# Optimization experiments

Hardware: AMD Instinct MI355X
Metric: run time of the kernel (lower is better)

The kernel has to match this reference:

```python
import jax, jax.numpy as jnp
import numpy as np

K = 64                      # sort-pool k
B_GRAPHS, N_PER = 256, 512  # graphs, nodes per graph
DIM_F, E_PER = 128, 8192    # node feature dim, edges per graph
EMB = 32


def setup_inputs() -> dict:
    key = jax.random.key(0)
    ks = jax.random.split(key, 12)
    N = B_GRAPHS * N_PER
    off = (jnp.arange(B_GRAPHS) * N_PER)[:, None]
    x = jax.random.normal(ks[0], (N, DIM_F), jnp.float32)
    edge_src = (jax.random.randint(ks[1], (B_GRAPHS, E_PER), 0, N_PER) + off).reshape(-1)
    edge_dst = (jax.random.randint(ks[2], (B_GRAPHS, E_PER), 0, N_PER) + off).reshape(-1)

    def lin(k, o, i):
        return (jax.random.normal(k, (o, i), jnp.float32) / np.float32(np.sqrt(i)))

    return {
        "x": x,
        "W0": lin(ks[3], EMB, DIM_F), "b0": jnp.zeros((EMB,), jnp.float32),
        "W1": lin(ks[4], EMB, EMB),   "b1": jnp.zeros((EMB,), jnp.float32),
        "W2": lin(ks[5], EMB, EMB),   "b2": jnp.zeros((EMB,), jnp.float32),
        "W3": lin(ks[6], 1, EMB),     "b3": jnp.zeros((1,), jnp.float32),
        "conv1_w": jax.random.normal(ks[7], (16, 1, 97), jnp.float32) / np.float32(np.sqrt(97.0)),
        "conv1_b": jnp.zeros((16,), jnp.float32),
        "conv2_w": jax.random.normal(ks[8], (32, 16, 5), jnp.float32) / np.float32(np.sqrt(80.0)),
        "conv2_b": jnp.zeros((32,), jnp.float32),
        "d1_w": lin(ks[9], 128, 896),  "d1_b": jnp.zeros((128,), jnp.float32),
        "d2_w": lin(ks[10], 10, 128),  "d2_b": jnp.zeros((10,), jnp.float32),
        "edge_src": edge_src, "edge_dst": edge_dst,
        "num_graphs": B_GRAPHS,
    }


def _dgcnn_conv(h_in, W, b, src, dst):
    # h = lin(x); message = (1/deg_src)[dst] * h[src]; scatter-add at dst
    N = h_in.shape[0]
    h = h_in @ W.T + b
    deg = jax.ops.segment_sum(jnp.ones_like(src, dtype=h.dtype), src, num_segments=N)
    norm = 1.0 / deg                       # self-loops guarantee deg >= 1
    msg = h[src] * norm[dst][:, None]      # [E+N, C]
    return jax.ops.segment_sum(msg, dst, num_segments=N)


def _forward(x, W0, b0, W1, b1, W2, b2, W3, b3,
             conv1_w, conv1_b, conv2_w, conv2_b,
             d1_w, d1_b, d2_w, d2_b, src, dst, num_graphs):
    N = x.shape[0]
    self_idx = jnp.arange(N)
    src = jnp.concatenate([src, self_idx])   # add_self_loops
    dst = jnp.concatenate([dst, self_idx])
    hs = []
    h = x
    for (W, b) in ((W0, b0), (W1, b1), (W2, b2), (W3, b3)):
        h = jnp.tanh(_dgcnn_conv(h, W, b, src, dst))
        hs.append(h)
    feat = jnp.concatenate(hs, axis=1)       # [N, 97]
    D = feat.shape[1]
    B = num_graphs
    n = N // B
    g = feat.reshape(B, n, D)
    # global_sort_pool: sort nodes per graph by last channel, descending, take top-k
    order = jnp.argsort(-g[:, :, -1], axis=1)[:, :K]
    topk = jnp.take_along_axis(g, order[:, :, None], axis=1)   # [B, K, D]
    # Conv1d(1,16,kernel=D,stride=D) over [B,1,K*D] == per-node linear on D
    c1 = jax.nn.relu(jnp.einsum('bkd,od->bok', topk, conv1_w[:, 0, :])
                     + conv1_b[None, :, None])                  # [B,16,K]
    p = c1.reshape(B, 16, K // 2, 2).max(axis=-1)               # MaxPool1d(2,2)
    c2 = jax.lax.conv_general_dilated(p, conv2_w, (1,), 'VALID',
                                      dimension_numbers=('NCH', 'OIH', 'NCH'))
    c2 = jax.nn.relu(c2 + conv2_b[None, :, None])               # [B,32,28]
    flat = c2.reshape(B, -1)                                    # [B,896]
    hid = jax.nn.relu(flat @ d1_w.T + d1_b)                     # dropout = identity (eval)
    return hid @ d2_w.T + d2_b                                  # [B,10]


def reference(x, W0, b0, W1, b1, W2, b2, W3, b3,
              conv1_w, conv1_b, conv2_w, conv2_b,
              d1_w, d1_b, d2_w, d2_b, edge_src, edge_dst, num_graphs):
    return _forward(x, W0, b0, W1, b1, W2, b2, W3, b3,
                    conv1_w, conv1_b, conv2_w, conv2_b,
                    d1_w, d1_b, d2_w, d2_b, edge_src, edge_dst, num_graphs)
```

## Files before the change

### kernel.cpp

```cpp
#include <hip/hip_runtime.h>

#define NG   256
#define NP   512
#define EPG  8192
#define FDIM 128
#define STB  36

#define OFF_STAGE 0
#define OFF_BUFB  65536
#define OFF_CSR   139264
#define OFF_OFFS  155648
#define OFF_WT    156680
#define OFF_CUR   156712
#define OFF_DCNT  158760
#define OFF_NRM   160808
#define SMEM_SZ   162856

#define OFF_KEY   OFF_CSR
#define OFF_RANKP (OFF_CSR + 2048)
#define OFF_TIDX  (OFF_CSR + 4096)
#define OFF_TKEY  (OFF_CSR + 4352)
#define OFF_L3    OFF_CUR
#define FO_FEAT 0
#define FO_C1   6208
#define FO_P    7232
#define FO_C2   7744
#define FO_HID  8640

__global__ __launch_bounds__(1024, 4) void dgcnn_fused(
    const float* __restrict__ x,
    const float* __restrict__ W0, const float* __restrict__ b0,
    const float* __restrict__ W1, const float* __restrict__ b1,
    const float* __restrict__ W2, const float* __restrict__ b2,
    const float* __restrict__ W3, const float* __restrict__ b3,
    const float* __restrict__ c1w, const float* __restrict__ c1b,
    const float* __restrict__ c2w, const float* __restrict__ c2b,
    const float* __restrict__ d1w, const float* __restrict__ d1b,
    const float* __restrict__ d2w, const float* __restrict__ d2b,
    const int* __restrict__ esrc, const int* __restrict__ edst,
    float* __restrict__ hs2,
    float* __restrict__ out)
{
  extern __shared__ char smem[];
  float*          stageF = (float*)(smem + OFF_STAGE);
  float*          bufB  = (float*)(smem + OFF_BUFB);
  unsigned short* csr   = (unsigned short*)(smem + OFF_CSR);
  unsigned short* offs  = (unsigned short*)(smem + OFF_OFFS);
  unsigned int*   wt    = (unsigned int*)(smem + OFF_WT);
  unsigned int*   cur   = (unsigned int*)(smem + OFF_CUR);
  unsigned int*   dcnt  = (unsigned int*)(smem + OFF_DCNT);
  float*          nrm   = (float*)(smem + OFF_NRM);
  float*          lin3S = (float*)(smem + OFF_L3);
  float*          keyA  = (float*)(smem + OFF_KEY);
  unsigned short* rankP = (unsigned short*)(smem + OFF_RANKP);
  unsigned short* topIdx= (unsigned short*)(smem + OFF_TIDX);
  float*          topKey= (float*)(smem + OFF_TKEY);

  const int g    = blockIdx.x;
  const int tid  = threadIdx.x;
  const int lane = tid & 63;
  const int wv   = __builtin_amdgcn_readfirstlane(tid >> 6);
  const int half = __builtin_amdgcn_readfirstlane(tid >> 9);
  const int v    = tid & 511;
  const int nb   = g * NP;

  const int ldRow0 = tid >> 3;
  const int ldGrp  = tid & 7;
  const int ldSwz  = (ldGrp ^ (ldRow0 & 7)) * 16;
  auto load_chunk = [&](int kc, float4* xr) {
    const float* base = x + (size_t)nb * FDIM + kc * 32 + ldGrp * 4;
#pragma unroll
    for (int it = 0; it < 4; it++)
      xr[it] = *(const float4*)(base + (size_t)(ldRow0 + it * 128) * FDIM);
  };
  auto store_chunk = [&](const float4* xr) {
#pragma unroll
    for (int it = 0; it < 4; it++)
      *(float4*)(smem + OFF_STAGE + (ldRow0 + it * 128) * 128 + ldSwz) = xr[it];
  };

  float4 xr[4], xr2[4];
  load_chunk(0, xr);
  const int eb = g * EPG;
  const int4* s4p = (const int4*)(esrc + eb);
  const int4* d4p = (const int4*)(edst + eb);
  const int4 sa = s4p[tid], sb = s4p[tid + 1024];
  const int4 da = d4p[tid], db = d4p[tid + 1024];

  int es[8], ed[8];
  es[0]=sa.x-nb; es[1]=sa.y-nb; es[2]=sa.z-nb; es[3]=sa.w-nb;
  es[4]=sb.x-nb; es[5]=sb.y-nb; es[6]=sb.z-nb; es[7]=sb.w-nb;
  ed[0]=da.x-nb; ed[1]=da.y-nb; ed[2]=da.z-nb; ed[3]=da.w-nb;
  ed[4]=db.x-nb; ed[5]=db.y-nb; ed[6]=db.z-nb; ed[7]=db.w-nb;

  if (tid < 512) { cur[tid] = 0u; dcnt[tid] = 0u; }

  float acc0[16];
#pragma unroll
  for (int c = 0; c < 16; c++) acc0[c] = b0[half * 16 + c];
  const char* rowp = smem + OFF_STAGE + v * 128;
  const int vswz = v & 7;

  auto compute_chunk = [&](const int kc) {
#pragma unroll
    for (int jg = 0; jg < 8; jg++) {
      const float4 t = *(const float4*)(rowp + ((jg ^ vswz) * 16));
#pragma unroll
      for (int c = 0; c < 16; c++) {
        const float* wr = W0 + (size_t)(half * 16 + c) * FDIM + kc * 32 + jg * 4;
        acc0[c] = fmaf(t.x, wr[0], acc0[c]);
        acc0[c] = fmaf(t.y, wr[1], acc0[c]);
        acc0[c] = fmaf(t.z, wr[2], acc0[c]);
        acc0[c] = fmaf(t.w, wr[3], acc0[c]);
      }
    }
  };

  __syncthreads();
  store_chunk(xr);
  load_chunk(1, xr2);
  __syncthreads();
#pragma unroll
  for (int i = 0; i < 8; i++) {
    atomicAdd(&dcnt[es[i]], 1u);
    atomicAdd(&dcnt[ed[i]], 65536u);
  }
  compute_chunk(0);
#pragma unroll
  for (int it = 0; it < 4; it++) xr[it] = xr2[it];
  __syncthreads();
  store_chunk(xr);
  load_chunk(2, xr2);
  __syncthreads();
  unsigned c_scan = 0;
  if (tid < 512) {
    const unsigned cw = dcnt[tid];
    nrm[tid] = 1.0f / (float)((cw & 0xFFFFu) + 1u);
    c_scan = cw >> 16;
    for (int d = 1; d < 64; d <<= 1) {
      const unsigned t = __shfl_up(c_scan, (unsigned)d, 64);
      if (lane >= d) c_scan += t;
    }
    if (lane == 63) wt[wv] = c_scan;
  }
  compute_chunk(1);
#pragma unroll
  for (int it = 0; it < 4; it++) xr[it] = xr2[it];
  __syncthreads();
  store_chunk(xr);
  load_chunk(3, xr2);
  __syncthreads();
  if (tid < 512) {
    unsigned base = 0;
    for (int w = 0; w < wv; w++) base += wt[w];
    offs[tid + 1] = (unsigned short)(base + c_scan);
    if (tid == 0) offs[0] = 0;
  }
  compute_chunk(2);
  __syncthreads();
  store_chunk(xr2);
  __syncthreads();
#pragma unroll
  for (int i = 0; i < 8; i++) {
    const unsigned pos = (unsigned)offs[ed[i]] + atomicAdd(&cur[ed[i]], 1u);
    csr[pos] = (unsigned short)es[i];
  }
  compute_chunk(3);
  {
    float4* br = (float4*)(bufB + v * STB + half * 16);
#pragma unroll
    for (int j = 0; j < 4; j++)
      br[j] = make_float4(acc0[j*4+0], acc0[j*4+1], acc0[j*4+2], acc0[j*4+3]);
  }
  __syncthreads();

  float h[16];
  auto do_agg = [&]() {
    float4 A0, A1, A2, A3;
    const float4* sr = (const float4*)(bufB + v * STB + half * 16);
    A0 = sr[0]; A1 = sr[1]; A2 = sr[2]; A3 = sr[3];
    const int e0 = offs[v], e1 = offs[v + 1];
    int e = e0;
    for (; e + 3 < e1; e += 4) {
      const int s0 = csr[e], s1 = csr[e + 1], s2 = csr[e + 2], s3 = csr[e + 3];
      const float4* rb0 = (const float4*)(bufB + s0 * STB + half * 16);
      const float4* rb1 = (const float4*)(bufB + s1 * STB + half * 16);
      const float4* rb2 = (const float4*)(bufB + s2 * STB + half * 16);
      const float4* rb3 = (const float4*)(bufB + s3 * STB + half * 16);
      const float4 p0 = rb0[0], p1 = rb0[1], p2 = rb0[2], p3 = rb0[3];
      const float4 q0 = rb1[0], q1 = rb1[1], q2 = rb1[2], q3 = rb1[3];
      const float4 r0 = rb2[0], r1 = rb2[1], r2 = rb2[2], r3 = rb2[3];
      const float4 t0 = rb3[0], t1 = rb3[1], t2 = rb3[2], t3 = rb3[3];
      A0.x += p0.x + q0.x; A0.y += p0.y + q0.y; A0.z += p0.z + q0.z; A0.w += p0.w + q0.w;
      A1.x += p1.x + q1.x; A1.y += p1.y + q1.y; A1.z += p1.z + q1.z; A1.w += p1.w + q1.w;
      A2.x += p2.x + q2.x; A2.y += p2.y + q2.y; A2.z += p2.z + q2.z; A2.w += p2.w + q2.w;
      A3.x += p3.x + q3.x; A3.y += p3.y + q3.y; A3.z += p3.z + q3.z; A3.w += p3.w + q3.w;
      A0.x += r0.x + t0.x; A0.y += r0.y + t0.y; A0.z += r0.z + t0.z; A0.w += r0.w + t0.w;
      A1.x += r1.x + t1.x; A1.y += r1.y + t1.y; A1.z += r1.z + t1.z; A1.w += r1.w + t1.w;
      A2.x += r2.x + t2.x; A2.y += r2.y + t2.y; A2.z += r2.z + t2.z; A2.w += r2.w + t2.w;
      A3.x += r3.x + t3.x; A3.y += r3.y + t3.y; A3.z += r3.z + t3.z; A3.w += r3.w + t3.w;
    }
    for (; e + 1 < e1; e += 2) {
      const int s0 = csr[e], s1 = csr[e + 1];
      const float4* rb0 = (const float4*)(bufB + s0 * STB + half * 16);
      const float4* rb1 = (const float4*)(bufB + s1 * STB + half * 16);
      const float4 p0 = rb0[0], p1 = rb0[1], p2 = rb0[2], p3 = rb0[3];
      const float4 q0 = rb1[0], q1 = rb1[1], q2 = rb1[2], q3 = rb1[3];
      A0.x += p0.x + q0.x; A0.y += p0.y + q0.y; A0.z += p0.z + q0.z; A0.w += p0.w + q0.w;
      A1.x += p1.x + q1.x; A1.y += p1.y + q1.y; A1.z += p1.z + q1.z; A1.w += p1.w + q1.w;
      A2.x += p2.x + q2.x; A2.y += p2.y + q2.y; A2.z += p2.z + q2.z; A2.w += p2.w + q2.w;
      A3.x += p3.x + q3.x; A3.y += p3.y + q3.y; A3.z += p3.z + q3.z; A3.w += p3.w + q3.w;
    }
    if (e < e1) {
      const int s = csr[e];
      const float4* rb = (const float4*)(bufB + s * STB + half * 16);
      const float4 r0 = rb[0], r1 = rb[1], r2 = rb[2], r3 = rb[3];
      A0.x += r0.x; A0.y += r0.y; A0.z += r0.z; A0.w += r0.w;
      A1.x += r1.x; A1.y += r1.y; A1.z += r1.z; A1.w += r1.w;
      A2.x += r2.x; A2.y += r2.y; A2.z += r2.z; A2.w += r2.w;
      A3.x += r3.x; A3.y += r3.y; A3.z += r3.z; A3.w += r3.w;
    }
    const float nv = nrm[v];
    h[0]=tanhf(A0.x*nv); h[1]=tanhf(A0.y*nv); h[2]=tanhf(A0.z*nv); h[3]=tanhf(A0.w*nv);
    h[4]=tanhf(A1.x*nv); h[5]=tanhf(A1.y*nv); h[6]=tanhf(A1.z*nv); h[7]=tanhf(A1.w*nv);
    h[8]=tanhf(A2.x*nv); h[9]=tanhf(A2.y*nv); h[10]=tanhf(A2.z*nv); h[11]=tanhf(A2.w*nv);
    h[12]=tanhf(A3.x*nv); h[13]=tanhf(A3.y*nv); h[14]=tanhf(A3.z*nv); h[15]=tanhf(A3.w*nv);
  };

  auto put_h = [&]() {
    float4* br = (float4*)(bufB + v * STB + half * 16);
#pragma unroll
    for (int j = 0; j < 4; j++)
      br[j] = make_float4(h[j*4+0], h[j*4+1], h[j*4+2], h[j*4+3]);
  };

  auto store_h1 = [&]() {
#pragma unroll
    for (int c = 0; c < 16; c++)
      stageF[(half * 16 + c) * 512 + v] = h[c];
  };

  auto spill2 = [&]() {
    float4* dst = (float4*)(hs2 + (size_t)(nb + v) * 32 + half * 16);
#pragma unroll
    for (int j = 0; j < 4; j++)
      dst[j] = make_float4(h[j*4+0], h[j*4+1], h[j*4+2], h[j*4+3]);
  };

  auto do_lin = [&](const float* __restrict__ W, const float* __restrict__ b) {
    float hf[32];
    const float4* rr = (const float4*)(bufB + v * STB);
#pragma unroll
    for (int j = 0; j < 8; j++) {
      const float4 t = rr[j];
      hf[j*4+0]=t.x; hf[j*4+1]=t.y; hf[j*4+2]=t.z; hf[j*4+3]=t.w;
    }
    __syncthreads();
    float acc[16];
#pragma unroll
    for (int c = 0; c < 16; c++) {
      const int C = half * 16 + c;
      const float* wr = W + C * 32;
      float a = b[C];
#pragma unroll
      for (int j = 0; j < 32; j++) a = fmaf(hf[j], wr[j], a);
      acc[c] = a;
    }
    float4* br = (float4*)(bufB + v * STB + half * 16);
#pragma unroll
    for (int j = 0; j < 4; j++)
      br[j] = make_float4(acc[j*4+0], acc[j*4+1], acc[j*4+2], acc[j*4+3]);
    __syncthreads();
  };

  do_agg();
  __syncthreads();
  put_h(); store_h1();
  __syncthreads();
  do_lin(W1, b1);
  do_agg();
  __syncthreads();
  put_h(); spill2();
  __syncthreads();
  do_lin(W2, b2);
  do_agg();
  __syncthreads();
  put_h();
  __syncthreads();

  if (tid < 512) {
    const float4* rr = (const float4*)(bufB + tid * STB);
    double a = (double)b3[0];
#pragma unroll
    for (int j = 0; j < 8; j++) {
      const float4 t = rr[j];
      a = fma((double)t.x, (double)W3[j*4+0], a);
      a = fma((double)t.y, (double)W3[j*4+1], a);
      a = fma((double)t.z, (double)W3[j*4+2], a);
      a = fma((double)t.w, (double)W3[j*4+3], a);
    }
    lin3S[tid] = (float)a;
  }
  __syncthreads();
  float h4 = 0.f;
  if (tid < 512) {
    double a = (double)lin3S[tid];
    const int e0 = offs[tid], e1 = offs[tid + 1];
    for (int e = e0; e < e1; e++) a += (double)lin3S[csr[e]];
    a *= (double)nrm[tid];
    h4 = tanhf((float)a);
  }
  __syncthreads();
  if (tid < 512) keyA[tid] = h4;
  __syncthreads();

  {
    const int i = tid & 511;
    const int p = tid >> 9;
    const float ki = keyA[i];
    const float4* k4 = (const float4*)(keyA + p * 256);
    int cnt = 0;
#pragma unroll 8
    for (int jj = 0; jj < 64; jj++) {
      const float4 kv = k4[jj];
      const int j0 = p * 256 + jj * 4;
      cnt += (kv.x > ki || (kv.x == ki && (j0    ) < i)) ? 1 : 0;
      cnt += (kv.y > ki || (kv.y == ki && (j0 + 1) < i)) ? 1 : 0;
      cnt += (kv.z > ki || (kv.z == ki && (j0 + 2) < i)) ? 1 : 0;
      cnt += (kv.w > ki || (kv.w == ki && (j0 + 3) < i)) ? 1 : 0;
    }
    rankP[tid] = (unsigned short)cnt;
  }
  __syncthreads();
  if (tid < 512) {
    const int r = (int)rankP[tid] + (int)rankP[tid + 512];
    if (r < 64) { topIdx[r] = (unsigned short)tid; topKey[r] = keyA[tid]; }
  }
  __syncthreads();

  {
    const int k = lane;
    const int t = wv;
    const int node = (int)topIdx[k];
    const float a0 = stageF[ t       * 512 + node];
    const float a1 = stageF[(t + 16) * 512 + node];
    const float* h2row = hs2 + (size_t)(nb + node) * 32;
    const float b0v = h2row[t];
    const float b1v = h2row[t + 16];
    const float* brow = bufB + node * STB;
    const float c0v = brow[t];
    const float c1v = brow[t + 16];
    const float kk = topKey[k];
    __syncthreads();
    float* featS = bufB + FO_FEAT;
    featS[ t        * 64 + k] = a0;
    featS[(t + 16)  * 64 + k] = a1;
    featS[(t + 32)  * 64 + k] = b0v;
    featS[(t + 48)  * 64 + k] = b1v;
    featS[(t + 64)  * 64 + k] = c0v;
    featS[(t + 80)  * 64 + k] = c1v;
    if (t == 0) featS[96 * 64 + k] = kk;
  }
  __syncthreads();

  {
    const float* featS = bufB + FO_FEAT;
    float* c1s = bufB + FO_C1;
    const int ch = wv;
    float a = c1b[ch];
    const float* wr = c1w + ch * 97;
    for (int d = 0; d < 97; d++)
      a = fmaf(featS[d * 64 + lane], wr[d], a);
    c1s[ch * 64 + lane] = fmaxf(a, 0.f);
  }
  __syncthreads();

  if (tid < 512) {
    const float* c1s = bufB + FO_C1;
    float* ps  = bufB + FO_P;
    const int o = tid >> 5, jj = tid & 31;
    ps[o * 32 + jj] = fmaxf(c1s[o * 64 + 2 * jj], c1s[o * 64 + 2 * jj + 1]);
  }
  __syncthreads();

  {
    const float* ps  = bufB + FO_P;
    float* c2s = bufB + FO_C2;
    const int o = wv;
    if (lane < 28) {
      float a0 = 0.f, a1 = 0.f;
      for (int i = 0; i < 16; i++) {
#pragma unroll
        for (int r = 0; r < 5; r++) {
          const float pv = ps[i * 32 + lane + r];
          a0 = fmaf(pv, c2w[((o     ) * 16 + i) * 5 + r], a0);
          a1 = fmaf(pv, c2w[((o + 16) * 16 + i) * 5 + r], a1);
        }
      }
      c2s[(o     ) * 28 + lane] = fmaxf(a0 + c2b[o     ], 0.f);
      c2s[(o + 16) * 28 + lane] = fmaxf(a1 + c2b[o + 16], 0.f);
    }
  }
  __syncthreads();

  {
    const float* c2s  = bufB + FO_C2;
    float* hids = bufB + FO_HID;
    float fl[14];
#pragma unroll
    for (int j = 0; j < 14; j++) fl[j] = c2s[lane + j * 64];
#pragma unroll 2
    for (int hh = 0; hh < 8; hh++) {
      const int hI = wv * 8 + hh;
      const float* wr = d1w + (size_t)hI * 896;
      float a = 0.f;
#pragma unroll
      for (int j = 0; j < 14; j++) a = fmaf(fl[j], wr[lane + j * 64], a);
#pragma unroll
      for (int m = 32; m > 0; m >>= 1) a += __shfl_xor(a, m, 64);
      if (lane == 0) hids[hI] = fmaxf(a + d1b[hI], 0.f);
    }
  }
  __syncthreads();

  if (tid < 10) {
    const float* hids = bufB + FO_HID;
    const float* wr = d2w + tid * 128;
    double a = (double)d2b[tid];
#pragma unroll 8
    for (int hh = 0; hh < 128; hh++) a = fma((double)hids[hh], (double)wr[hh], a);
    out[g * 10 + tid] = (float)a;
  }
}

extern "C" void kernel_launch(void* const* d_in, const int* in_sizes, int n_in,
                              void* d_out, int out_size, void* d_ws, size_t ws_size,
                              hipStream_t stream) {
  const float* x   = (const float*)d_in[0];
  const float* W0  = (const float*)d_in[1];
  const float* b0  = (const float*)d_in[2];
  const float* W1  = (const float*)d_in[3];
  const float* b1  = (const float*)d_in[4];
  const float* W2  = (const float*)d_in[5];
  const float* b2  = (const float*)d_in[6];
  const float* W3  = (const float*)d_in[7];
  const float* b3  = (const float*)d_in[8];
  const float* c1w = (const float*)d_in[9];
  const float* c1b = (const float*)d_in[10];
  const float* c2w = (const float*)d_in[11];
  const float* c2b = (const float*)d_in[12];
  const float* d1w = (const float*)d_in[13];
  const float* d1b = (const float*)d_in[14];
  const float* d2w = (const float*)d_in[15];
  const float* d2b = (const float*)d_in[16];
  const int* esrc  = (const int*)d_in[17];
  const int* edst  = (const int*)d_in[18];

  float* hs2 = (float*)d_ws;
  float* outp = (float*)d_out;

  hipFuncSetAttribute(reinterpret_cast<const void*>(dgcnn_fused),
                      hipFuncAttributeMaxDynamicSharedMemorySize, SMEM_SZ);
  dgcnn_fused<<<NG, 1024, SMEM_SZ, stream>>>(x, W0, b0, W1, b1, W2, b2, W3, b3,
                                             c1w, c1b, c2w, c2b, d1w, d1b, d2w, d2b,
                                             esrc, edst, hs2, outp);
}
```

Measured before the change: 281.2 us.

## Drop put_h round trips and barriers; fuse maxpool into conv1 via shuffles

The layer-1 and layer-2 linear steps now read their inputs directly from the transposed stage buffer and from the global hs2 spill, instead of writing them into bufB and reading them back. This removes put_h calls and several __syncthreads. The key buffer is moved to a separate shared-memory region so the final tanh can write it directly, which drops one more barrier. The conv1 ReLU and the MaxPool are combined using wavefront shuffles, which removes the c1 shared-memory buffer and a barrier, at the cost of uncached global reads for the layer-2 input.

```diff
diff --git a/kernel.cpp b/kernel.cpp
--- a/kernel.cpp
+++ b/kernel.cpp
@@ -12,20 +12,20 @@
 #define OFF_OFFS  155648
 #define OFF_WT    156680
 #define OFF_CUR   156712
-#define OFF_DCNT  158760
-#define OFF_NRM   160808
-#define SMEM_SZ   162856
-
-#define OFF_KEY   OFF_CSR
-#define OFF_RANKP (OFF_CSR + 2048)
-#define OFF_TIDX  (OFF_CSR + 4096)
-#define OFF_TKEY  (OFF_CSR + 4352)
+#define OFF_PAD   158760
+#define OFF_DCNT  158768
+#define OFF_NRM   160816
+#define SMEM_SZ   162864
+
 #define OFF_L3    OFF_CUR
+#define OFF_KEY   OFF_DCNT
+#define OFF_RANKP OFF_CSR
+#define OFF_TIDX  (OFF_CSR + 2048)
+#define OFF_TKEY  (OFF_CSR + 2304)
 #define FO_FEAT 0
-#define FO_C1   6208
-#define FO_P    7232
-#define FO_C2   7744
-#define FO_HID  8640
+#define FO_P    6208
+#define FO_C2   6720
+#define FO_HID  7616
 
 __global__ __launch_bounds__(1024, 4) void dgcnn_fused(
     const float* __restrict__ x,
@@ -247,15 +247,7 @@
       dst[j] = make_float4(h[j*4+0], h[j*4+1], h[j*4+2], h[j*4+3]);
   };
 
-  auto do_lin = [&](const float* __restrict__ W, const float* __restrict__ b) {
-    float hf[32];
-    const float4* rr = (const float4*)(bufB + v * STB);
-#pragma unroll
-    for (int j = 0; j < 8; j++) {
-      const float4 t = rr[j];
-      hf[j*4+0]=t.x; hf[j*4+1]=t.y; hf[j*4+2]=t.z; hf[j*4+3]=t.w;
-    }
-    __syncthreads();
+  auto lin_core = [&](const float* hf, const float* __restrict__ W, const float* __restrict__ b) {
     float acc[16];
 #pragma unroll
     for (int c = 0; c < 16; c++) {
@@ -270,19 +262,32 @@
 #pragma unroll
     for (int j = 0; j < 4; j++)
       br[j] = make_float4(acc[j*4+0], acc[j*4+1], acc[j*4+2], acc[j*4+3]);
-    __syncthreads();
   };
 
   do_agg();
-  __syncthreads();
-  put_h(); store_h1();
-  __syncthreads();
-  do_lin(W1, b1);
+  store_h1();
+  __syncthreads();
+  {
+    float hf[32];
+#pragma unroll
+    for (int j = 0; j < 32; j++) hf[j] = stageF[j * 512 + v];
+    lin_core(hf, W1, b1);
+  }
+  __syncthreads();
   do_agg();
-  __syncthreads();
-  put_h(); spill2();
-  __syncthreads();
-  do_lin(W2, b2);
+  spill2();
+  __syncthreads();
+  {
+    float hf[32];
+    const float4* rr = (const float4*)(hs2 + (size_t)(nb + v) * 32);
+#pragma unroll
+    for (int j = 0; j < 8; j++) {
+      const float4 t = rr[j];
+      hf[4*j]=t.x; hf[4*j+1]=t.y; hf[4*j+2]=t.z; hf[4*j+3]=t.w;
+    }
+    lin_core(hf, W2, b2);
+  }
+  __syncthreads();
   do_agg();
   __syncthreads();
   put_h();
@@ -302,16 +307,13 @@
     lin3S[tid] = (float)a;
   }
   __syncthreads();
-  float h4 = 0.f;
   if (tid < 512) {
     double a = (double)lin3S[tid];
     const int e0 = offs[tid], e1 = offs[tid + 1];
     for (int e = e0; e < e1; e++) a += (double)lin3S[csr[e]];
     a *= (double)nrm[tid];
-    h4 = tanhf((float)a);
-  }
-  __syncthreads();
-  if (tid < 512) keyA[tid] = h4;
+    keyA[tid] = tanhf((float)a);
+  }
   __syncthreads();
 
   {
@@ -365,21 +367,16 @@
 
   {
     const float* featS = bufB + FO_FEAT;
-    float* c1s = bufB + FO_C1;
+    float* ps = bufB + FO_P;
     const int ch = wv;
     float a = c1b[ch];
     const float* wr = c1w + ch * 97;
     for (int d = 0; d < 97; d++)
       a = fmaf(featS[d * 64 + lane], wr[d], a);
-    c1s[ch * 64 + lane] = fmaxf(a, 0.f);
-  }
-  __syncthreads();
-
-  if (tid < 512) {
-    const float* c1s = bufB + FO_C1;
-    float* ps  = bufB + FO_P;
-    const int o = tid >> 5, jj = tid & 31;
-    ps[o * 32 + jj] = fmaxf(c1s[o * 64 + 2 * jj], c1s[o * 64 + 2 * jj + 1]);
+    a = fmaxf(a, 0.f);
+    const float m  = fmaxf(a, __shfl_down(a, 1, 64));
+    const float pv = __shfl(m, (lane & 31) * 2, 64);
+    if (lane < 32) ps[ch * 32 + lane] = pv;
   }
   __syncthreads();
 
```

Result: no change. 276.5 us (-1.7%).
